# Performance work log

Measured on AMD Instinct MI355X. Metric: run time of the kernel, lower is better.

Reference implementation:

```python
import jax, jax.numpy as jnp
import numpy as np

H = 16  # n_heads
EPS = 1e-12  # torch F.normalize eps


def setup_inputs() -> dict:
    key = jax.random.key(0)
    ks = jax.random.split(key, 7)
    dim = 1024
    b, n = 8, 4096
    s = 1.0 / np.sqrt(dim)
    return {
        "x": jax.random.normal(ks[0], (b, n, dim), dtype=jnp.float32),
        "Wq": jax.random.normal(ks[1], (dim, dim), dtype=jnp.float32) * s,
        "Wk": jax.random.normal(ks[2], (dim, dim), dtype=jnp.float32) * s,
        "Wv": jax.random.normal(ks[3], (dim, dim), dtype=jnp.float32) * s,
        "scale": jnp.ones((H, 1, 1), dtype=jnp.float32),
        "Wo": jax.random.normal(ks[4], (dim, dim), dtype=jnp.float32) * s,
        "bo": jnp.zeros((dim,), dtype=jnp.float32),
    }


def _l2norm(t):
    # F.normalize(t, dim=-1, p=2): t / max(||t||_2, eps)
    nrm = jnp.sqrt(jnp.sum(t * t, axis=-1, keepdims=True))
    return t / jnp.maximum(nrm, EPS)


def reference(x, Wq, Wk, Wv, scale, Wo, bo):
    b, n, c = x.shape
    d = c // H

    def proj_t(W):
        # Linear (x @ W.T) -> [b, n, h, d] -> transposed layout [b, h, d, n]
        return (x @ W.T).reshape(b, n, H, d).transpose(0, 2, 3, 1)

    q = _l2norm(proj_t(Wq))  # [b, h, d, n], L2-normalized over tokens
    k = _l2norm(proj_t(Wk))
    v = proj_t(Wv)

    # cross-covariance attention over channel dim: [b, h, d, d]
    attn = jnp.einsum('bhdn,bhen->bhde', k, q) * scale
    attn = jax.nn.softmax(attn, axis=-1)
    out = jnp.einsum('bhde,bhen->bhdn', attn, v)  # [b, h, d, n]

    # faithful to torch: raw view of contiguous [b, h, d, n] into [b, n, c]
    out = out.reshape(b, n, c)
    return out @ Wo.T + bo
```

## Files before the change

### kernel.cpp

```cpp
#include <hip/hip_runtime.h>
#include <stdint.h>


typedef unsigned short u16;
typedef __attribute__((ext_vector_type(8))) short bf16x8;
typedef __attribute__((ext_vector_type(8))) u16 u16x8;
typedef __attribute__((ext_vector_type(4))) u16 u16x4;
typedef __attribute__((ext_vector_type(4))) float f32x4;

__device__ __forceinline__ float bf2f(u16 u) {
  union { unsigned int i; float f; } x;
  x.i = ((unsigned int)u) << 16;
  return x.f;
}
__device__ __forceinline__ u16 f2bf(float f) {
  union { float f; unsigned int i; } x;
  x.f = f;
  unsigned int u = x.i;
  u = u + 0x7fffu + ((u >> 16) & 1u);
  return (u16)(u >> 16);
}

__device__ __forceinline__ void gload16(const u16* g, u16* l) {
  __builtin_amdgcn_global_load_lds(
      (const __attribute__((address_space(1))) void*)g,
      (__attribute__((address_space(3))) void*)l, 16, 0, 0);
}

__global__ __launch_bounds__(256) void cast_kernel(
    const float4* __restrict__ x, const float4* __restrict__ wq,
    const float4* __restrict__ wk, const float4* __restrict__ wv,
    const float4* __restrict__ wo, u16x4* __restrict__ xbf,
    u16x4* __restrict__ wbf) {
  long i = (long)blockIdx.x * 256 + threadIdx.x;
  float4 v = x[i];
  u16x4 o;
  o[0] = f2bf(v.x); o[1] = f2bf(v.y); o[2] = f2bf(v.z); o[3] = f2bf(v.w);
  xbf[i] = o;
  if (i < 1048576) {
    int sel = (int)(i >> 18);
    const float4* s = (sel == 0) ? wq : (sel == 1) ? wk : (sel == 2) ? wv : wo;
    float4 w = s[i & 262143];
    u16x4 ow;
    ow[0] = f2bf(w.x); ow[1] = f2bf(w.y); ow[2] = f2bf(w.z); ow[3] = f2bf(w.w);
    wbf[i] = ow;
  }
}

template <int MODE>
__global__ __launch_bounds__(256) void gemm_nt(const u16* __restrict__ A,
                                               const u16* __restrict__ B,
                                               void* __restrict__ C,
                                               const float* __restrict__ bias) {
  __shared__ u16 As[128 * 32];
  __shared__ u16 Bs[128 * 32];
  const int tid = threadIdx.x;
  const int lane = tid & 63;
  const int wave = tid >> 6;
  const int wm = (wave & 1) * 64;
  const int wn = (wave >> 1) * 64;
  const int m0 = blockIdx.y * 128;
  const int n0 = blockIdx.x * 128;

  long aoff, boff, coff;
  if (MODE == 0) {
    int w = blockIdx.z >> 3;
    int b = blockIdx.z & 7;
    aoff = (long)w * 1048576;
    boff = (long)b * 4194304;
    coff = (long)blockIdx.z * 4194304;
  } else {
    aoff = (long)blockIdx.z * 4194304;
    boff = 0;
    coff = (long)blockIdx.z * 4194304;
  }

  const u16* Ag = A + aoff + (long)(m0 + (tid >> 2)) * 1024 + (tid & 3) * 8;
  const u16* Bg = B + boff + (long)(n0 + (tid >> 2)) * 1024 + (tid & 3) * 8;
  u16* Asw = As + tid * 8;
  u16* Bsw = Bs + tid * 8;

  f32x4 acc[4][4];
  const f32x4 z4 = {0.f, 0.f, 0.f, 0.f};
#pragma unroll
  for (int i = 0; i < 4; i++)
#pragma unroll
    for (int j = 0; j < 4; j++) acc[i][j] = z4;

  const int fm = lane & 15;
  const int fk = (lane >> 4) * 8;

  for (int kt = 0; kt < 1024; kt += 32) {
    __syncthreads();
    gload16(Ag + kt, Asw);
    gload16(Ag + kt + 64 * 1024, Asw + 64 * 32);
    gload16(Bg + kt, Bsw);
    gload16(Bg + kt + 64 * 1024, Bsw + 64 * 32);
    __syncthreads();
    bf16x8 af[4], bfm[4];
#pragma unroll
    for (int i = 0; i < 4; i++)
      af[i] = *(const bf16x8*)&As[(wm + i * 16 + fm) * 32 + fk];
#pragma unroll
    for (int j = 0; j < 4; j++)
      bfm[j] = *(const bf16x8*)&Bs[(wn + j * 16 + fm) * 32 + fk];
#pragma unroll
    for (int i = 0; i < 4; i++)
#pragma unroll
      for (int j = 0; j < 4; j++)
        acc[i][j] = __builtin_amdgcn_mfma_f32_16x16x32_bf16(af[i], bfm[j],
                                                            acc[i][j], 0, 0, 0);
  }

  const int rq = (lane >> 4) * 4;
  if (MODE == 1) {
    float* Cf = (float*)C + coff;
#pragma unroll
    for (int j = 0; j < 4; j++) {
      float bv = bias[n0 + wn + j * 16 + fm];
#pragma unroll
      for (int i = 0; i < 4; i++)
#pragma unroll
        for (int r = 0; r < 4; r++) {
          int m = m0 + wm + i * 16 + rq + r;
          int n = n0 + wn + j * 16 + fm;
          Cf[(long)m * 1024 + n] = acc[i][j][r] + bv;
        }
    }
  } else {
    const int ldc = (MODE == 0) ? 4096 : 1024;
    u16* Cb = (u16*)C + coff;
#pragma unroll
    for (int i = 0; i < 4; i++)
#pragma unroll
      for (int j = 0; j < 4; j++)
#pragma unroll
        for (int r = 0; r < 4; r++) {
          int m = m0 + wm + i * 16 + rq + r;
          int n = n0 + wn + j * 16 + fm;
          Cb[(long)m * ldc + n] = f2bf(acc[i][j][r]);
        }
  }
}

__global__ __launch_bounds__(256) void attn_partial(const u16* __restrict__ qk,
                                                    float* __restrict__ attnP,
                                                    float* __restrict__ nsqP) {
  const int bh = blockIdx.x;
  const int b = bh >> 4, h = bh & 15;
  const int tid = threadIdx.x, lane = tid & 63, wave = tid >> 6;
  const int sl = blockIdx.y * 4 + wave;
  const u16* Qg = qk + (long)b * 4194304 + (long)h * 64 * 4096;
  const u16* Kg = Qg + 33554432L;

  const int fm = lane & 15;
  const long kbase = (long)sl * 256 + (lane >> 4) * 8;

  f32x4 acc[4][4];
  const f32x4 z4 = {0.f, 0.f, 0.f, 0.f};
#pragma unroll
  for (int i = 0; i < 4; i++)
#pragma unroll
    for (int j = 0; j < 4; j++) acc[i][j] = z4;
  float sk[4] = {0.f, 0.f, 0.f, 0.f}, sq[4] = {0.f, 0.f, 0.f, 0.f};

  for (int kt = 0; kt < 256; kt += 32) {
    bf16x8 ak[4], aq[4];
#pragma unroll
    for (int i = 0; i < 4; i++) {
      ak[i] = *(const bf16x8*)(Kg + (long)(i * 16 + fm) * 4096 + kbase + kt);
      aq[i] = *(const bf16x8*)(Qg + (long)(i * 16 + fm) * 4096 + kbase + kt);
    }
#pragma unroll
    for (int i = 0; i < 4; i++) {
      const u16x8 kv = (u16x8)ak[i], qv = (u16x8)aq[i];
#pragma unroll
      for (int e = 0; e < 8; e++) {
        float fkk = bf2f(kv[e]); sk[i] += fkk * fkk;
        float fq = bf2f(qv[e]);  sq[i] += fq * fq;
      }
    }
#pragma unroll
    for (int i = 0; i < 4; i++)
#pragma unroll
      for (int j = 0; j < 4; j++)
        acc[i][j] = __builtin_amdgcn_mfma_f32_16x16x32_bf16(ak[i], aq[j],
                                                            acc[i][j], 0, 0, 0);
  }

#pragma unroll
  for (int i = 0; i < 4; i++) {
    sk[i] += __shfl_xor(sk[i], 16); sk[i] += __shfl_xor(sk[i], 32);
    sq[i] += __shfl_xor(sq[i], 16); sq[i] += __shfl_xor(sq[i], 32);
  }
  float* np = nsqP + ((long)sl * 128 + bh) * 128;
  if (lane < 16) {
#pragma unroll
    for (int i = 0; i < 4; i++) {
      np[i * 16 + lane] = sk[i];
      np[64 + i * 16 + lane] = sq[i];
    }
  }
  float* sp = attnP + ((long)sl * 128 + bh) * 4096;
  const int rq = (lane >> 4) * 4;
#pragma unroll
  for (int i = 0; i < 4; i++)
#pragma unroll
    for (int j = 0; j < 4; j++)
#pragma unroll
      for (int r = 0; r < 4; r++)
        sp[(i * 16 + rq + r) * 64 + j * 16 + fm] = acc[i][j][r];
}

__global__ __launch_bounds__(128) void attn_finalize(const float* __restrict__ attnP,
                                                     const float* __restrict__ nsqP,
                                                     const float* __restrict__ scale,
                                                     u16* __restrict__ attnb) {
  const int bh = blockIdx.x;
  const int h = bh & 15;
  const int tid = threadIdx.x;
  __shared__ float rn[2][64];
  {
    int which = tid >> 6, row = tid & 63;
    float s = 0.f;
#pragma unroll
    for (int sl = 0; sl < 16; sl++)
      s += nsqP[((long)sl * 128 + bh) * 128 + which * 64 + row];
    rn[which][row] = 1.0f / fmaxf(sqrtf(s), 1e-12f);
  }
  __syncthreads();
  if (tid < 64) {
    const int d = tid;
    float row[64];
#pragma unroll
    for (int e = 0; e < 64; e++) row[e] = 0.f;
    for (int sl = 0; sl < 16; sl++) {
      const float4* p =
          (const float4*)(attnP + ((long)sl * 128 + bh) * 4096 + d * 64);
#pragma unroll
      for (int e4 = 0; e4 < 16; e4++) {
        float4 v = p[e4];
        row[e4 * 4 + 0] += v.x;
        row[e4 * 4 + 1] += v.y;
        row[e4 * 4 + 2] += v.z;
        row[e4 * 4 + 3] += v.w;
      }
    }
    const float rk = rn[0][d] * scale[h];
    float mx = -1e30f;
#pragma unroll
    for (int e = 0; e < 64; e++) {
      row[e] = row[e] * rk * rn[1][e];
      mx = fmaxf(mx, row[e]);
    }
    float sum = 0.f;
#pragma unroll
    for (int e = 0; e < 64; e++) {
      row[e] = __expf(row[e] - mx);
      sum += row[e];
    }
    float inv = 1.0f / sum;
    u16* out = attnb + ((long)bh * 64 + d) * 64;
#pragma unroll
    for (int e = 0; e < 64; e++) out[e] = f2bf(row[e] * inv);
  }
}

__global__ __launch_bounds__(256) void av_mfma(const u16* __restrict__ attnb,
                                               const u16* __restrict__ vt,
                                               u16* __restrict__ outb) {
  const int bh = blockIdx.y;
  const int b = bh >> 4, h = bh & 15;
  const int n0 = blockIdx.x * 256;
  const int tid = threadIdx.x, lane = tid & 63, wave = tid >> 6;
  __shared__ u16 As[64 * 72];
  {
    const u16* src = attnb + (long)bh * 4096 + (tid >> 2) * 64 + (tid & 3) * 16;
    u16x8 v0 = *(const u16x8*)src;
    u16x8 v1 = *(const u16x8*)(src + 8);
    u16* dst = As + (tid >> 2) * 72 + (tid & 3) * 16;
    *(u16x8*)dst = v0;
    *(u16x8*)(dst + 8) = v1;
  }
  __syncthreads();
  const int fm = lane & 15;
  const int fe = (lane >> 4) * 8;
  const u16* Vg = vt + (long)b * 4194304 + h * 64 + fe;

  f32x4 acc[4][4];
  const f32x4 z4 = {0.f, 0.f, 0.f, 0.f};
#pragma unroll
  for (int i = 0; i < 4; i++)
#pragma unroll
    for (int j = 0; j < 4; j++) acc[i][j] = z4;

  bf16x8 af[4][2];
#pragma unroll
  for (int i = 0; i < 4; i++)
#pragma unroll
    for (int ks = 0; ks < 2; ks++)
      af[i][ks] = *(const bf16x8*)&As[(i * 16 + fm) * 72 + fe + ks * 32];

#pragma unroll
  for (int ks = 0; ks < 2; ks++)
#pragma unroll
    for (int j = 0; j < 4; j++) {
      int n = n0 + wave * 64 + j * 16 + fm;
      bf16x8 bf = *(const bf16x8*)(Vg + (long)n * 1024 + ks * 32);
#pragma unroll
      for (int i = 0; i < 4; i++)
        acc[i][j] = __builtin_amdgcn_mfma_f32_16x16x32_bf16(af[i][ks], bf,
                                                            acc[i][j], 0, 0, 0);
    }

  const int rq = (lane >> 4) * 4;
  u16* Ob = outb + ((long)b * 1024 + h * 64) * 4096;
#pragma unroll
  for (int i = 0; i < 4; i++)
#pragma unroll
    for (int j = 0; j < 4; j++)
#pragma unroll
      for (int r = 0; r < 4; r++) {
        int d = i * 16 + rq + r;
        int n = n0 + wave * 64 + j * 16 + fm;
        Ob[(long)d * 4096 + n] = f2bf(acc[i][j][r]);
      }
}

extern "C" void kernel_launch(void* const* d_in, const int* in_sizes, int n_in,
                              void* d_out, int out_size, void* d_ws, size_t ws_size,
                              hipStream_t stream) {
  const float* x = (const float*)d_in[0];
  const float* Wq = (const float*)d_in[1];
  const float* Wk = (const float*)d_in[2];
  const float* Wv = (const float*)d_in[3];
  const float* scale = (const float*)d_in[4];
  const float* Wo = (const float*)d_in[5];
  const float* bo = (const float*)d_in[6];
  float* out = (float*)d_out;

  u16* xbf = (u16*)d_ws;
  u16* wbf = xbf + 33554432;
  u16* qk = wbf + 4194304;
  u16* vt = qk + 67108864;
  float* attnP = (float*)(vt + 33554432);
  float* nsqP = attnP + 8388608;
  u16* attnb = (u16*)(nsqP + 262144);
  u16* outb = qk;

  cast_kernel<<<32768, 256, 0, stream>>>((const float4*)x, (const float4*)Wq,
                                         (const float4*)Wk, (const float4*)Wv,
                                         (const float4*)Wo, (u16x4*)xbf,
                                         (u16x4*)wbf);
  gemm_nt<0><<<dim3(32, 8, 16), 256, 0, stream>>>(wbf, xbf, (void*)qk, nullptr);
  gemm_nt<2><<<dim3(8, 32, 8), 256, 0, stream>>>(xbf, wbf + 2 * 1048576,
                                                 (void*)vt, nullptr);
  attn_partial<<<dim3(128, 4), 256, 0, stream>>>(qk, attnP, nsqP);
  attn_finalize<<<128, 128, 0, stream>>>(attnP, nsqP, scale, attnb);
  av_mfma<<<dim3(16, 128), 256, 0, stream>>>(attnb, vt, outb);
  gemm_nt<1><<<dim3(8, 32, 8), 256, 0, stream>>>(outb, wbf + 3 * 1048576,
                                                 (void*)out, bo);
}
```

Measured before the change: 687.8 us.

## Replace 128x128 GEMM with 256x256 double-buffered swizzled LDS pipeline

Swaps the simple 128x128 tile bf16 GEMM, which synchronised twice per 32-wide k step, for a 256x256 tile, 512-thread kernel. It uses 64-wide k tiles, double-buffered LDS with XOR swizzling, and staggered global-to-LDS prefetch interleaved with MFMA quarters under explicit waitcnt and barriers. The aim is to raise arithmetic intensity, hide global load latency and avoid LDS bank conflicts in all three projection GEMMs. The cost is 128KB of LDS per block, heavy register use and fragile hand-tuned waitcnt ordering.

```diff
diff --git a/kernel.cpp b/kernel.cpp
--- a/kernel.cpp
+++ b/kernel.cpp
@@ -47,20 +47,94 @@
   }
 }
 
+
+#define STG(Lb, G, r0, kt)                                                   \
+  gload16((G) + (long)((r0) + rl) * 1024 + (kt) * 64 + slswz,                \
+          (Lb) + (r0) * 64 + tid * 8)
+
+#define LDB(Bb)                                                              \
+  _Pragma("unroll") for (int jj = 0; jj < 4; ++jj)                           \
+  _Pragma("unroll") for (int ks = 0; ks < 2; ++ks) {                         \
+    const int idx = (wc * 64 + jj * 16 + fm) * 64 + ks * 32 + fk;            \
+    bfr[jj][ks] = *(const bf16x8*)((Bb) + (idx ^ swz));                      \
+  }
+
+#define LDA(Ab, qr)                                                          \
+  _Pragma("unroll") for (int i = 0; i < 4; ++i)                              \
+  _Pragma("unroll") for (int ks = 0; ks < 2; ++ks) {                         \
+    const int idx = (wr * 128 + (qr)*64 + i * 16 + fm) * 64 + ks * 32 + fk;  \
+    afr[i][ks] = *(const bf16x8*)((Ab) + (idx ^ swz));                       \
+  }
+
+#define MM(qr, qc)                                                           \
+  {                                                                          \
+    __builtin_amdgcn_s_setprio(1);                                           \
+    _Pragma("unroll") for (int ks = 0; ks < 2; ++ks)                         \
+    _Pragma("unroll") for (int i = 0; i < 4; ++i)                            \
+    _Pragma("unroll") for (int jj = 0; jj < 2; ++jj)                         \
+        acc[(qr)*4 + i][(qc)*2 + jj] =                                       \
+            __builtin_amdgcn_mfma_f32_16x16x32_bf16(                         \
+                afr[i][ks], bfr[(qc)*2 + jj][ks],                            \
+                acc[(qr)*4 + i][(qc)*2 + jj], 0, 0, 0);                      \
+    __builtin_amdgcn_s_setprio(0);                                           \
+  }
+
+#define LGKM0                                        \
+  do {                                               \
+    asm volatile("s_waitcnt lgkmcnt(0)" ::: "memory"); \
+    __builtin_amdgcn_sched_barrier(0);               \
+  } while (0)
+#define VM6 asm volatile("s_waitcnt vmcnt(6)" ::: "memory")
+#define VM0 asm volatile("s_waitcnt vmcnt(0)" ::: "memory")
+#define VMNONE (void)0
+#define BAR __builtin_amdgcn_s_barrier()
+
+#define TILE(Ab, Bb, Aoth, kt, S1, S2, VMW)                                  \
+  {                                                                          \
+          \
+    LDB(Bb);                                                                 \
+    LDA(Ab, 0);                                                              \
+    if (S1) { STG(Aoth, Ag, 128, (kt) + 1); STG(Aoth, Ag, 192, (kt) + 1); }  \
+    BAR;                                                                     \
+    MM(0, 0);                                                                \
+    LGKM0;                                                                   \
+    BAR;                                                                     \
+                   \
+    if (S2) { STG(Bb, Bg, 0, (kt) + 2); STG(Bb, Bg, 64, (kt) + 2); }         \
+    BAR;                                                                     \
+    MM(0, 1);                                                                \
+    BAR;                                                                     \
+                                      \
+    LDA(Ab, 1);                                                              \
+    if (S2) { STG(Bb, Bg, 128, (kt) + 2); STG(Bb, Bg, 192, (kt) + 2); }      \
+    BAR;                                                                     \
+    MM(1, 0);                                                                \
+    LGKM0;                                                                   \
+    BAR;                                                                     \
+                                                   \
+    if (S2) { STG(Ab, Ag, 0, (kt) + 2); STG(Ab, Ag, 64, (kt) + 2); }         \
+    BAR;                                                                     \
+    MM(1, 1);                                                                \
+    VMW;                                                                     \
+    BAR;                                                                     \
+  }
+
 template <int MODE>
-__global__ __launch_bounds__(256) void gemm_nt(const u16* __restrict__ A,
-                                               const u16* __restrict__ B,
-                                               void* __restrict__ C,
-                                               const float* __restrict__ bias) {
-  __shared__ u16 As[128 * 32];
-  __shared__ u16 Bs[128 * 32];
+__global__ __launch_bounds__(512, 2) void gemm256(const u16* __restrict__ A,
+                                                  const u16* __restrict__ B,
+                                                  void* __restrict__ C,
+                                                  const float* __restrict__ bias) {
+  __shared__ u16 As0[16384];
+  __shared__ u16 As1[16384];
+  __shared__ u16 Bs0[16384];
+  __shared__ u16 Bs1[16384];
   const int tid = threadIdx.x;
   const int lane = tid & 63;
   const int wave = tid >> 6;
-  const int wm = (wave & 1) * 64;
-  const int wn = (wave >> 1) * 64;
-  const int m0 = blockIdx.y * 128;
-  const int n0 = blockIdx.x * 128;
+  const int wr = wave >> 2;
+  const int wc = wave & 3;
+  const int m0 = blockIdx.y * 256;
+  const int n0 = blockIdx.x * 256;
 
   long aoff, boff, coff;
   if (MODE == 0) {
@@ -74,71 +148,71 @@
     boff = 0;
     coff = (long)blockIdx.z * 4194304;
   }
-
-  const u16* Ag = A + aoff + (long)(m0 + (tid >> 2)) * 1024 + (tid & 3) * 8;
-  const u16* Bg = B + boff + (long)(n0 + (tid >> 2)) * 1024 + (tid & 3) * 8;
-  u16* Asw = As + tid * 8;
-  u16* Bsw = Bs + tid * 8;
-
-  f32x4 acc[4][4];
+  const u16* Ag = A + aoff + (long)m0 * 1024;
+  const u16* Bg = B + boff + (long)n0 * 1024;
+
+  const int rl = tid >> 3;
+  const int slswz = ((tid & 7) ^ (rl & 7)) * 8;
+  const int fm = lane & 15;
+  const int fk = (lane >> 4) << 3;
+  const int swz = (fm & 7) << 3;
+
+  f32x4 acc[8][4];
   const f32x4 z4 = {0.f, 0.f, 0.f, 0.f};
 #pragma unroll
-  for (int i = 0; i < 4; i++)
+  for (int i = 0; i < 8; i++)
 #pragma unroll
     for (int j = 0; j < 4; j++) acc[i][j] = z4;
 
-  const int fm = lane & 15;
-  const int fk = (lane >> 4) * 8;
-
-  for (int kt = 0; kt < 1024; kt += 32) {
-    __syncthreads();
-    gload16(Ag + kt, Asw);
-    gload16(Ag + kt + 64 * 1024, Asw + 64 * 32);
-    gload16(Bg + kt, Bsw);
-    gload16(Bg + kt + 64 * 1024, Bsw + 64 * 32);
-    __syncthreads();
-    bf16x8 af[4], bfm[4];
-#pragma unroll
-    for (int i = 0; i < 4; i++)
-      af[i] = *(const bf16x8*)&As[(wm + i * 16 + fm) * 32 + fk];
-#pragma unroll
-    for (int j = 0; j < 4; j++)
-      bfm[j] = *(const bf16x8*)&Bs[(wn + j * 16 + fm) * 32 + fk];
-#pragma unroll
-    for (int i = 0; i < 4; i++)
-#pragma unroll
-      for (int j = 0; j < 4; j++)
-        acc[i][j] = __builtin_amdgcn_mfma_f32_16x16x32_bf16(af[i], bfm[j],
-                                                            acc[i][j], 0, 0, 0);
-  }
+  bf16x8 afr[4][2], bfr[4][2];
+
+  STG(Bs0, Bg, 0, 0);   STG(Bs0, Bg, 64, 0);
+  STG(Bs0, Bg, 128, 0); STG(Bs0, Bg, 192, 0);
+  STG(As0, Ag, 0, 0);   STG(As0, Ag, 64, 0);
+  STG(As0, Ag, 128, 0); STG(As0, Ag, 192, 0);
+  STG(Bs1, Bg, 0, 1);   STG(Bs1, Bg, 64, 1);
+  STG(Bs1, Bg, 128, 1); STG(Bs1, Bg, 192, 1);
+  STG(As1, Ag, 0, 1);   STG(As1, Ag, 64, 1);
+  VM6;
+  BAR;
+
+#pragma unroll 1
+  for (int it = 0; it < 7; ++it) {
+    TILE(As0, Bs0, As1, 2 * it, true, true, VM6);
+    TILE(As1, Bs1, As0, 2 * it + 1, true, true, VM6);
+  }
+  TILE(As0, Bs0, As1, 14, true, false, VM0);
+  TILE(As1, Bs1, As0, 15, false, false, VMNONE);
 
   const int rq = (lane >> 4) * 4;
+  const int mBase = m0 + wr * 128;
+  const int nBase = n0 + wc * 64;
   if (MODE == 1) {
     float* Cf = (float*)C + coff;
 #pragma unroll
-    for (int j = 0; j < 4; j++) {
-      float bv = bias[n0 + wn + j * 16 + fm];
-#pragma unroll
-      for (int i = 0; i < 4; i++)
-#pragma unroll
-        for (int r = 0; r < 4; r++) {
-          int m = m0 + wm + i * 16 + rq + r;
-          int n = n0 + wn + j * 16 + fm;
-          Cf[(long)m * 1024 + n] = acc[i][j][r] + bv;
+    for (int jj = 0; jj < 4; ++jj) {
+      float bv = bias[nBase + jj * 16 + fm];
+#pragma unroll
+      for (int i = 0; i < 8; ++i)
+#pragma unroll
+        for (int r = 0; r < 4; ++r) {
+          int m = mBase + i * 16 + rq + r;
+          int n = nBase + jj * 16 + fm;
+          Cf[(long)m * 1024 + n] = acc[i][jj][r] + bv;
         }
     }
   } else {
     const int ldc = (MODE == 0) ? 4096 : 1024;
     u16* Cb = (u16*)C + coff;
 #pragma unroll
-    for (int i = 0; i < 4; i++)
-#pragma unroll
-      for (int j = 0; j < 4; j++)
-#pragma unroll
-        for (int r = 0; r < 4; r++) {
-          int m = m0 + wm + i * 16 + rq + r;
-          int n = n0 + wn + j * 16 + fm;
-          Cb[(long)m * ldc + n] = f2bf(acc[i][j][r]);
+    for (int i = 0; i < 8; ++i)
+#pragma unroll
+      for (int jj = 0; jj < 4; ++jj)
+#pragma unroll
+        for (int r = 0; r < 4; ++r) {
+          int m = mBase + i * 16 + rq + r;
+          int n = nBase + jj * 16 + fm;
+          Cb[(long)m * ldc + n] = f2bf(acc[i][jj][r]);
         }
   }
 }
@@ -352,12 +426,12 @@
                                          (const float4*)Wk, (const float4*)Wv,
                                          (const float4*)Wo, (u16x4*)xbf,
                                          (u16x4*)wbf);
-  gemm_nt<0><<<dim3(32, 8, 16), 256, 0, stream>>>(wbf, xbf, (void*)qk, nullptr);
-  gemm_nt<2><<<dim3(8, 32, 8), 256, 0, stream>>>(xbf, wbf + 2 * 1048576,
+  gemm256<0><<<dim3(16, 4, 16), 512, 0, stream>>>(wbf, xbf, (void*)qk, nullptr);
+  gemm256<2><<<dim3(4, 16, 8), 512, 0, stream>>>(xbf, wbf + 2 * 1048576,
                                                  (void*)vt, nullptr);
   attn_partial<<<dim3(128, 4), 256, 0, stream>>>(qk, attnP, nsqP);
   attn_finalize<<<128, 128, 0, stream>>>(attnP, nsqP, scale, attnb);
   av_mfma<<<dim3(16, 128), 256, 0, stream>>>(attnb, vt, outb);
-  gemm_nt<1><<<dim3(8, 32, 8), 256, 0, stream>>>(outb, wbf + 3 * 1048576,
+  gemm256<1><<<dim3(4, 16, 8), 512, 0, stream>>>(outb, wbf + 3 * 1048576,
                                                  (void*)out, bo);
 }
```

Measured after the change: 624.3 us. 9.2% less time.
